# Performance work log

Measured on AMD Instinct MI355X. Metric: run time of the kernel, lower is better.

Reference implementation:

```python
import jax, jax.numpy as jnp
import numpy as np

NUM_FEATS = 40
FEAT_EMB_DIM = 16
MARK_DIM = 1024
HIDDEN = 4096
BATCH = 16384


def setup_inputs() -> dict:
    key = jax.random.key(0)
    ks = jax.random.split(key, 9)
    in_dim = NUM_FEATS * FEAT_EMB_DIM + 2 * MARK_DIM
    return {
        "emb_i": jax.random.normal(ks[0], (BATCH, MARK_DIM), dtype=jnp.float32),
        "emb_a": jax.random.normal(ks[1], (BATCH, MARK_DIM), dtype=jnp.float32),
        "feat_mask": jax.random.randint(ks[2], (BATCH, NUM_FEATS), 0, 2, dtype=jnp.int32),
        "feat_on_embs": jax.random.normal(ks[3], (NUM_FEATS, FEAT_EMB_DIM), dtype=jnp.float32),
        "feat_off_embs": jax.random.normal(ks[4], (NUM_FEATS, FEAT_EMB_DIM), dtype=jnp.float32),
        "W1": jax.random.normal(ks[5], (HIDDEN, in_dim), dtype=jnp.float32) / np.sqrt(in_dim),
        "b1": jax.random.normal(ks[6], (HIDDEN,), dtype=jnp.float32) * 0.01,
        "W2": jax.random.normal(ks[7], (1, HIDDEN), dtype=jnp.float32) / np.sqrt(HIDDEN),
        "b2": jax.random.normal(ks[8], (1,), dtype=jnp.float32) * 0.01,
    }


def reference(emb_i, emb_a, feat_mask, feat_on_embs, feat_off_embs, W1, b1, W2, b2):
    # Per-feature embedding select: index == position, so on/off tables broadcast
    # over batch; mask picks on-emb where feature is positive. [B, F, E]
    feats = jnp.where(feat_mask[:, :, None] > 0,
                      feat_on_embs[None, :, :],
                      feat_off_embs[None, :, :])
    B = emb_i.shape[0]
    concat = jnp.concatenate(
        [emb_i, emb_a, feats.reshape(B, -1)], axis=-1)  # [B, 2*D + F*E]
    h = jax.nn.relu(concat @ W1.T + b1)                 # [B, HIDDEN]
    return h @ W2.T + b2                                # [B, 1]
```

## Files before the change

### kernel.cpp

```cpp
#include <hip/hip_runtime.h>
#include <hip/hip_bf16.h>
#include <stdint.h>

#define BATCH 16384
#define MARK  1024
#define NF    40
#define FE    16
#define KDIM  2688
#define HID   4096
#define BK    32
#define KT    (KDIM / BK)

typedef __bf16 bf16x8 __attribute__((ext_vector_type(8)));
typedef float  f32x4  __attribute__((ext_vector_type(4)));

static __device__ __forceinline__ unsigned short f2bf(float f) {
  union { float f; uint32_t u; } v; v.f = f;
  uint32_t u = v.u;
  uint32_t r = (u + 0x7FFFu + ((u >> 16) & 1u)) >> 16;
  return (unsigned short)r;
}

__global__ __launch_bounds__(256) void build_concat(
    const float* __restrict__ emb_i, const float* __restrict__ emb_a,
    const int* __restrict__ mask, const float* __restrict__ fon,
    const float* __restrict__ foff, unsigned short* __restrict__ out) {
  const int b = blockIdx.x;
  const float4* ri = (const float4*)(emb_i + (size_t)b * MARK);
  const float4* ra = (const float4*)(emb_a + (size_t)b * MARK);
  const int* mrow = mask + b * NF;
  unsigned short* orow = out + (size_t)b * KDIM;
  for (int g = threadIdx.x; g < KDIM / 4; g += 256) {
    const int base = g * 4;
    float4 v;
    if (base < MARK) {
      v = ri[g];
    } else if (base < 2 * MARK) {
      v = ra[g - MARK / 4];
    } else {
      const int idx = base - 2 * MARK;
      const int f = idx >> 4;
      const float* tab = (mrow[f] > 0) ? fon : foff;
      v = *(const float4*)(tab + f * FE + (idx & 15));
    }
    ushort4 o;
    o.x = f2bf(v.x); o.y = f2bf(v.y); o.z = f2bf(v.z); o.w = f2bf(v.w);
    *(ushort4*)(orow + base) = o;
  }
}

__global__ __launch_bounds__(256) void convert_w1(
    const float* __restrict__ w, unsigned short* __restrict__ o, int n4) {
  const int stride = gridDim.x * 256;
  for (int i = blockIdx.x * 256 + threadIdx.x; i < n4; i += stride) {
    float4 v = ((const float4*)w)[i];
    ushort4 u;
    u.x = f2bf(v.x); u.y = f2bf(v.y); u.z = f2bf(v.z); u.w = f2bf(v.w);
    ((ushort4*)o)[i] = u;
  }
}

__global__ __launch_bounds__(256) void out_init(float* __restrict__ out,
                                                const float* __restrict__ b2) {
  const int i = blockIdx.x * 256 + threadIdx.x;
  if (i < BATCH) out[i] = b2[0];
}

#define GL16(g, l)                                                              \
  __builtin_amdgcn_global_load_lds(                                             \
      (const __attribute__((address_space(1))) void*)(g),                       \
      (__attribute__((address_space(3))) void*)(l), 16, 0, 0)

__global__ __launch_bounds__(256, 2) void gemm_fused(
    const unsigned short* __restrict__ A,
    const unsigned short* __restrict__ Wb,
    const float* __restrict__ b1,
    const float* __restrict__ w2,
    float* __restrict__ out) {
  __shared__ unsigned short lds_a[2][128 * BK];
  __shared__ unsigned short lds_b[2][128 * BK];

  const int tid  = threadIdx.x;
  const int wid  = tid >> 6;
  const int lane = tid & 63;

  const int bid    = blockIdx.x;
  const int tile_n = bid & 31;
  const int tile_m = bid >> 5;

  const int srow  = (wid << 5) + (lane >> 2);
  const int skoff = (lane & 3) * 8;
  const unsigned short* pA0 = A + (size_t)(tile_m * 128 + srow) * KDIM + skoff;
  const unsigned short* pA1 = pA0 + (size_t)16 * KDIM;
  const unsigned short* pB0 = Wb + (size_t)(tile_n * 128 + srow) * KDIM + skoff;
  const unsigned short* pB1 = pB0 + (size_t)16 * KDIM;
  const int lco = wid * 1024;

  GL16(pA0, &lds_a[0][lco]);
  GL16(pA1, &lds_a[0][lco + 512]);
  GL16(pB0, &lds_b[0][lco]);
  GL16(pB1, &lds_b[0][lco + 512]);
  pA0 += BK; pA1 += BK; pB0 += BK; pB1 += BK;

  const int wave_m = wid >> 1, wave_n = wid & 1;
  const int fr = lane & 15, k8 = lane >> 4;
  const int aoff = (wave_m * 64 + fr) * BK + k8 * 8;
  const int boff = (wave_n * 64 + fr) * BK + k8 * 8;

  f32x4 acc[4][4];
#pragma unroll
  for (int m = 0; m < 4; ++m)
#pragma unroll
    for (int n = 0; n < 4; ++n) acc[m][n] = (f32x4){0.f, 0.f, 0.f, 0.f};

  int buf = 0;
  for (int kt = 0; kt < KT; ++kt) {
    __syncthreads();
    if (kt + 1 < KT) {
      GL16(pA0, &lds_a[buf ^ 1][lco]);
      GL16(pA1, &lds_a[buf ^ 1][lco + 512]);
      GL16(pB0, &lds_b[buf ^ 1][lco]);
      GL16(pB1, &lds_b[buf ^ 1][lco + 512]);
      pA0 += BK; pA1 += BK; pB0 += BK; pB1 += BK;
    }
    bf16x8 af[4], bfr[4];
#pragma unroll
    for (int m = 0; m < 4; ++m)
      af[m] = *reinterpret_cast<const bf16x8*>(&lds_a[buf][aoff + m * 16 * BK]);
#pragma unroll
    for (int n = 0; n < 4; ++n)
      bfr[n] = *reinterpret_cast<const bf16x8*>(&lds_b[buf][boff + n * 16 * BK]);
#pragma unroll
    for (int m = 0; m < 4; ++m)
#pragma unroll
      for (int n = 0; n < 4; ++n)
        acc[m][n] = __builtin_amdgcn_mfma_f32_16x16x32_bf16(af[m], bfr[n],
                                                            acc[m][n], 0, 0, 0);
    buf ^= 1;
  }

  float b1v[4], w2v[4];
  const int gcol_base = tile_n * 128 + wave_n * 64 + fr;
#pragma unroll
  for (int n = 0; n < 4; ++n) {
    b1v[n] = b1[gcol_base + n * 16];
    w2v[n] = w2[gcol_base + n * 16];
  }
  const int grow_base = tile_m * 128 + wave_m * 64 + k8 * 4;
#pragma unroll
  for (int m = 0; m < 4; ++m) {
    float vs[4] = {0.f, 0.f, 0.f, 0.f};
#pragma unroll
    for (int n = 0; n < 4; ++n) {
      f32x4 a = acc[m][n];
#pragma unroll
      for (int j = 0; j < 4; ++j) {
        float h = a[j] + b1v[n];
        h = h > 0.f ? h : 0.f;
        vs[j] = fmaf(h, w2v[n], vs[j]);
      }
    }
#pragma unroll
    for (int j = 0; j < 4; ++j) {
      vs[j] += __shfl_xor(vs[j], 1, 16);
      vs[j] += __shfl_xor(vs[j], 2, 16);
      vs[j] += __shfl_xor(vs[j], 4, 16);
      vs[j] += __shfl_xor(vs[j], 8, 16);
    }
    if (fr == 0) {
#pragma unroll
      for (int j = 0; j < 4; ++j)
        atomicAdd(&out[grow_base + m * 16 + j], vs[j]);
    }
  }
}

extern "C" void kernel_launch(void* const* d_in, const int* in_sizes, int n_in,
                              void* d_out, int out_size, void* d_ws, size_t ws_size,
                              hipStream_t stream) {
  const float* emb_i = (const float*)d_in[0];
  const float* emb_a = (const float*)d_in[1];
  const int*   fmask = (const int*)d_in[2];
  const float* fon   = (const float*)d_in[3];
  const float* foff  = (const float*)d_in[4];
  const float* W1    = (const float*)d_in[5];
  const float* b1    = (const float*)d_in[6];
  const float* W2    = (const float*)d_in[7];
  const float* b2    = (const float*)d_in[8];
  float* out = (float*)d_out;

  unsigned short* concat = (unsigned short*)d_ws;
  unsigned short* w1b    = concat + (size_t)BATCH * KDIM;

  build_concat<<<BATCH, 256, 0, stream>>>(emb_i, emb_a, fmask, fon, foff, concat);
  convert_w1<<<2048, 256, 0, stream>>>(W1, w1b, HID * KDIM / 4);
  out_init<<<BATCH / 256, 256, 0, stream>>>(out, b2);
  gemm_fused<<<(BATCH / 128) * (HID / 128), 256, 0, stream>>>(concat, w1b, b1,
                                                              W2, out);
}
```

Before: 602.7 us.

## Rewrite fused GEMM with 256x256 tiles, 8 waves, swizzled LDS and interleaved staging

The bf16 MFMA GEMM moves from 128x128 tiles with 4 waves and BK=32 to 256x256 tiles with 8 waves and BK=64. The K loop is restructured into quarter-tile phases that interleave global-to-LDS staging with MFMA work, using XOR-swizzled LDS layouts, explicit waitcnt and barriers, and s_setprio around MFMA blocks. Partial row sums are reduced in shared memory before a single atomic per row, which cuts global atomics. The aim is higher arithmetic intensity per loaded byte and better overlap of memory with compute, at the cost of much higher register and LDS pressure, plus fragile hand-placed synchronisation.

Measured after the change: 541.6 us. 10.1% less time.

```diff
diff --git a/kernel.cpp b/kernel.cpp
--- a/kernel.cpp
+++ b/kernel.cpp
@@ -8,8 +8,8 @@
 #define FE    16
 #define KDIM  2688
 #define HID   4096
-#define BK    32
-#define KT    (KDIM / BK)
+#define BK    64
+#define NKT   (KDIM / BK)
 
 typedef __bf16 bf16x8 __attribute__((ext_vector_type(8)));
 typedef float  f32x4  __attribute__((ext_vector_type(4)));
@@ -71,107 +71,176 @@
       (const __attribute__((address_space(1))) void*)(g),                       \
       (__attribute__((address_space(3))) void*)(l), 16, 0, 0)
 
-__global__ __launch_bounds__(256, 2) void gemm_fused(
+#define BAR()        __builtin_amdgcn_s_barrier()
+#define WAIT_LGKM0() asm volatile("s_waitcnt lgkmcnt(0)" ::: "memory")
+#define WAIT_VM6()   asm volatile("s_waitcnt vmcnt(6)" ::: "memory")
+
+__global__ __launch_bounds__(512, 2) void gemm_fused(
     const unsigned short* __restrict__ A,
     const unsigned short* __restrict__ Wb,
     const float* __restrict__ b1,
     const float* __restrict__ w2,
     float* __restrict__ out) {
-  __shared__ unsigned short lds_a[2][128 * BK];
-  __shared__ unsigned short lds_b[2][128 * BK];
+  __shared__ unsigned short sA[2][256 * BK];
+  __shared__ unsigned short sB[2][256 * BK];
+  __shared__ float spart[2][4][128];
 
   const int tid  = threadIdx.x;
   const int wid  = tid >> 6;
   const int lane = tid & 63;
-
-  const int bid    = blockIdx.x;
-  const int tile_n = bid & 31;
-  const int tile_m = bid >> 5;
-
-  const int srow  = (wid << 5) + (lane >> 2);
-  const int skoff = (lane & 3) * 8;
-  const unsigned short* pA0 = A + (size_t)(tile_m * 128 + srow) * KDIM + skoff;
-  const unsigned short* pA1 = pA0 + (size_t)16 * KDIM;
-  const unsigned short* pB0 = Wb + (size_t)(tile_n * 128 + srow) * KDIM + skoff;
-  const unsigned short* pB1 = pB0 + (size_t)16 * KDIM;
-  const int lco = wid * 1024;
-
-  GL16(pA0, &lds_a[0][lco]);
-  GL16(pA1, &lds_a[0][lco + 512]);
-  GL16(pB0, &lds_b[0][lco]);
-  GL16(pB1, &lds_b[0][lco + 512]);
-  pA0 += BK; pA1 += BK; pB0 += BK; pB1 += BK;
-
-  const int wave_m = wid >> 1, wave_n = wid & 1;
-  const int fr = lane & 15, k8 = lane >> 4;
-  const int aoff = (wave_m * 64 + fr) * BK + k8 * 8;
-  const int boff = (wave_n * 64 + fr) * BK + k8 * 8;
-
-  f32x4 acc[4][4];
-#pragma unroll
-  for (int m = 0; m < 4; ++m)
-#pragma unroll
-    for (int n = 0; n < 4; ++n) acc[m][n] = (f32x4){0.f, 0.f, 0.f, 0.f};
-
-  int buf = 0;
-  for (int kt = 0; kt < KT; ++kt) {
-    __syncthreads();
-    if (kt + 1 < KT) {
-      GL16(pA0, &lds_a[buf ^ 1][lco]);
-      GL16(pA1, &lds_a[buf ^ 1][lco + 512]);
-      GL16(pB0, &lds_b[buf ^ 1][lco]);
-      GL16(pB1, &lds_b[buf ^ 1][lco + 512]);
-      pA0 += BK; pA1 += BK; pB0 += BK; pB1 += BK;
-    }
-    bf16x8 af[4], bfr[4];
-#pragma unroll
-    for (int m = 0; m < 4; ++m)
-      af[m] = *reinterpret_cast<const bf16x8*>(&lds_a[buf][aoff + m * 16 * BK]);
-#pragma unroll
-    for (int n = 0; n < 4; ++n)
-      bfr[n] = *reinterpret_cast<const bf16x8*>(&lds_b[buf][boff + n * 16 * BK]);
-#pragma unroll
-    for (int m = 0; m < 4; ++m)
-#pragma unroll
-      for (int n = 0; n < 4; ++n)
-        acc[m][n] = __builtin_amdgcn_mfma_f32_16x16x32_bf16(af[m], bfr[n],
-                                                            acc[m][n], 0, 0, 0);
-    buf ^= 1;
-  }
+  const int fr   = lane & 15;
+  const int k8   = lane >> 4;
+  const int wm   = wid >> 2;
+  const int wn   = wid & 3;
+
+  const int tile_n = blockIdx.x & 15;
+  const int tile_m = blockIdx.x >> 4;
+
+  const int lrow = lane >> 3;
+  const int lsrc = ((lane & 7) ^ lrow) * 8;
+  const unsigned short* Aptr =
+      A + ((size_t)tile_m * 256 + lrow) * KDIM + lsrc;
+  const unsigned short* Bptr =
+      Wb + ((size_t)tile_n * 256 + lrow) * KDIM + lsrc;
+
+  const int swz0 = ((k8 ^ (fr & 7)) * 8);
+  const int swz1 = (((4 + k8) ^ (fr & 7)) * 8);
+
+#define STAGEA(BUF, MH, KT)                                                    \
+  { _Pragma("unroll") for (int g = 0; g < 2; ++g) {                            \
+      const int r0 = g * 128 + (MH)*64 + wid * 8;                              \
+      GL16(Aptr + (size_t)r0 * KDIM + (KT)*BK, &sA[BUF][r0 * BK]); } }
+
+#define STAGEB(BUF, NH, KT)                                                    \
+  { _Pragma("unroll") for (int g = 0; g < 2; ++g) {                            \
+      const int r0 = g * 128 + (wid >> 2) * 64 + (NH)*32 + (wid & 3) * 8;      \
+      GL16(Bptr + (size_t)r0 * KDIM + (KT)*BK, &sB[BUF][r0 * BK]); } }
+
+#define LOADA(BUF, MH)                                                         \
+  { _Pragma("unroll") for (int i = 0; i < 4; ++i) {                            \
+      const unsigned short* p =                                                \
+          &sA[BUF][(wm * 128 + (MH)*64 + i * 16 + fr) * BK];                   \
+      af[i][0] = *(const bf16x8*)(p + swz0);                                   \
+      af[i][1] = *(const bf16x8*)(p + swz1); } }
+
+#define LOADB(BUF, NH)                                                         \
+  { _Pragma("unroll") for (int j = 0; j < 2; ++j) {                            \
+      const unsigned short* p =                                                \
+          &sB[BUF][(wn * 64 + (NH)*32 + j * 16 + fr) * BK];                    \
+      bfr[j][0] = *(const bf16x8*)(p + swz0);                                  \
+      bfr[j][1] = *(const bf16x8*)(p + swz1); } }
+
+#define MMA(MH, NH)                                                            \
+  { __builtin_amdgcn_s_setprio(1);                                             \
+    _Pragma("unroll") for (int i = 0; i < 4; ++i)                              \
+    _Pragma("unroll") for (int j = 0; j < 2; ++j) {                            \
+      acc[(MH)*4 + i][(NH)*2 + j] = __builtin_amdgcn_mfma_f32_16x16x32_bf16(   \
+          af[i][0], bfr[j][0], acc[(MH)*4 + i][(NH)*2 + j], 0, 0, 0);          \
+      acc[(MH)*4 + i][(NH)*2 + j] = __builtin_amdgcn_mfma_f32_16x16x32_bf16(   \
+          af[i][1], bfr[j][1], acc[(MH)*4 + i][(NH)*2 + j], 0, 0, 0); }        \
+    __builtin_amdgcn_s_setprio(0); }
+
+  f32x4 acc[8][4];
+#pragma unroll
+  for (int i = 0; i < 8; ++i)
+#pragma unroll
+    for (int j = 0; j < 4; ++j) acc[i][j] = (f32x4){0.f, 0.f, 0.f, 0.f};
+  bf16x8 af[4][2], bfr[2][2];
 
   float b1v[4], w2v[4];
-  const int gcol_base = tile_n * 128 + wave_n * 64 + fr;
-#pragma unroll
-  for (int n = 0; n < 4; ++n) {
-    b1v[n] = b1[gcol_base + n * 16];
-    w2v[n] = w2[gcol_base + n * 16];
-  }
-  const int grow_base = tile_m * 128 + wave_m * 64 + k8 * 4;
-#pragma unroll
-  for (int m = 0; m < 4; ++m) {
-    float vs[4] = {0.f, 0.f, 0.f, 0.f};
-#pragma unroll
-    for (int n = 0; n < 4; ++n) {
-      f32x4 a = acc[m][n];
+  const int gcol = tile_n * 256 + wn * 64 + fr;
+#pragma unroll
+  for (int j = 0; j < 4; ++j) {
+    b1v[j] = b1[gcol + j * 16];
+    w2v[j] = w2[gcol + j * 16];
+  }
+
+  STAGEA(0, 0, 0); STAGEB(0, 1, 0); STAGEA(0, 1, 0); STAGEB(0, 0, 0);
+  STAGEA(1, 0, 1); STAGEB(1, 1, 1); STAGEA(1, 1, 1);
+  WAIT_VM6();
+  BAR();
+
+#pragma unroll 1
+  for (int t = 0; t < NKT; t += 2) {
+    int t2 = t + 2; if (t2 >= NKT) t2 -= NKT;
+    int t3 = t + 3; if (t3 >= NKT) t3 -= NKT;
+    LOADA(0, 0); LOADB(0, 0);
+    STAGEB(1, 0, t + 1);
+    BAR(); WAIT_LGKM0();
+    MMA(0, 0);
+    BAR();
+    LOADB(0, 1);
+    STAGEA(0, 0, t2);
+    BAR(); WAIT_LGKM0();
+    MMA(0, 1);
+    BAR();
+    LOADA(0, 1);
+    STAGEB(0, 1, t2);
+    BAR(); WAIT_LGKM0();
+    MMA(1, 1);
+    BAR();
+    LOADB(0, 0);
+    STAGEA(0, 1, t2);
+    BAR(); WAIT_LGKM0();
+    MMA(1, 0);
+    WAIT_VM6();
+    BAR();
+    LOADA(1, 0); LOADB(1, 0);
+    STAGEB(0, 0, t2);
+    BAR(); WAIT_LGKM0();
+    MMA(0, 0);
+    BAR();
+    LOADB(1, 1);
+    STAGEA(1, 0, t3);
+    BAR(); WAIT_LGKM0();
+    MMA(0, 1);
+    BAR();
+    LOADA(1, 1);
+    STAGEB(1, 1, t3);
+    BAR(); WAIT_LGKM0();
+    MMA(1, 1);
+    BAR();
+    LOADB(1, 0);
+    STAGEA(1, 1, t3);
+    BAR(); WAIT_LGKM0();
+    MMA(1, 0);
+    WAIT_VM6();
+    BAR();
+  }
+
+#pragma unroll
+  for (int i = 0; i < 8; ++i) {
+    float vs[4];
+#pragma unroll
+    for (int r = 0; r < 4; ++r) {
+      float s = 0.f;
 #pragma unroll
       for (int j = 0; j < 4; ++j) {
-        float h = a[j] + b1v[n];
+        float h = acc[i][j][r] + b1v[j];
         h = h > 0.f ? h : 0.f;
-        vs[j] = fmaf(h, w2v[n], vs[j]);
+        s = fmaf(h, w2v[j], s);
       }
-    }
-#pragma unroll
-    for (int j = 0; j < 4; ++j) {
-      vs[j] += __shfl_xor(vs[j], 1, 16);
-      vs[j] += __shfl_xor(vs[j], 2, 16);
-      vs[j] += __shfl_xor(vs[j], 4, 16);
-      vs[j] += __shfl_xor(vs[j], 8, 16);
+      vs[r] = s;
+    }
+#pragma unroll
+    for (int r = 0; r < 4; ++r) {
+      vs[r] += __shfl_xor(vs[r], 1, 16);
+      vs[r] += __shfl_xor(vs[r], 2, 16);
+      vs[r] += __shfl_xor(vs[r], 4, 16);
+      vs[r] += __shfl_xor(vs[r], 8, 16);
     }
     if (fr == 0) {
 #pragma unroll
-      for (int j = 0; j < 4; ++j)
-        atomicAdd(&out[grow_base + m * 16 + j], vs[j]);
-    }
+      for (int r = 0; r < 4; ++r)
+        spart[wm][wn][i * 16 + k8 * 4 + r] = vs[r];
+    }
+  }
+  __syncthreads();
+  if (tid < 256) {
+    const int rl = tid & 127, wmr = tid >> 7;
+    float s = spart[wmr][0][rl] + spart[wmr][1][rl] +
+              spart[wmr][2][rl] + spart[wmr][3][rl];
+    atomicAdd(&out[(size_t)tile_m * 256 + tid], s);
   }
 }
 
@@ -195,6 +264,6 @@
   build_concat<<<BATCH, 256, 0, stream>>>(emb_i, emb_a, fmask, fon, foff, concat);
   convert_w1<<<2048, 256, 0, stream>>>(W1, w1b, HID * KDIM / 4);
   out_init<<<BATCH / 256, 256, 0, stream>>>(out, b2);
-  gemm_fused<<<(BATCH / 128) * (HID / 128), 256, 0, stream>>>(concat, w1b, b1,
+  gemm_fused<<<(BATCH / 256) * (HID / 256), 512, 0, stream>>>(concat, w1b, b1,
                                                               W2, out);
 }
```
